# Kernel tuning notes

Hardware: AMD Instinct MI355X
Metric: run time of the kernel (lower is better)

## Reference

```python
import jax, jax.numpy as jnp
import numpy as np
from jax import lax

HID = 512
NEG = -1e30

def conv2d(x, w, pad):
    # x: [N,C,H,W], w: [O,I,kh,kw]
    return lax.conv_general_dilated(x, w, (1, 1), [(pad, pad), (pad, pad)],
                                    dimension_numbers=('NCHW', 'OIHW', 'NCHW'))

def maxpool3s2p1(x):
    return lax.reduce_window(x, -jnp.inf, lax.max, (1, 1, 3, 3), (1, 1, 2, 2),
                             [(0, 0), (0, 0), (1, 1), (1, 1)])

def setup_inputs() -> dict:
    key = jax.random.key(0)
    ks = jax.random.split(key, 12)
    N, B = 128, 16
    gid = jnp.repeat(jnp.arange(B), N // B).astype(jnp.float32)  # sorted group ids
    rois = jnp.concatenate([gid[:, None], jax.random.uniform(ks[0], (N, 4))], axis=1)
    interact_feat = jax.random.normal(ks[1], (N, 2304, 1, 16, 16), jnp.float32)
    bbox_feat = jax.random.normal(ks[2], (N, 1024, 4, 7, 7), jnp.float32)
    s = lambda k, sh: jax.random.normal(k, sh, jnp.float32) * 0.02
    return {
        'rois': rois,
        'interact_feat': interact_feat,
        'bbox_feat': bbox_feat,
        'w_reduce': s(ks[3], (HID, 2304, 1, 1)),
        'w_rsize': s(ks[4], (HID, HID, 3, 3)),
        'wq': s(ks[5], (HID, HID, 3, 3)),
        'wk': s(ks[6], (HID, HID, 3, 3)),
        'wv': s(ks[7], (HID, HID, 3, 3)),
        'w1': s(ks[8], (HID, HID, 3, 3)),
        'gamma': jnp.ones((HID,), jnp.float32),
        'beta': jnp.zeros((HID,), jnp.float32),
        'w_fc': s(ks[9], (HID, 2 * HID)),
    }

def reference(rois, interact_feat, bbox_feat, w_reduce, w_rsize, wq, wk, wv, w1, gamma, beta, w_fc):
    f = interact_feat[:, :, 0]                      # squeeze(2): [N,2304,16,16]
    f = jax.nn.relu(conv2d(f, w_reduce, 0))         # [N,512,16,16]
    f = conv2d(f, w_rsize, 0)                       # no padding -> [N,512,14,14]
    f = maxpool3s2p1(f)                             # [N,512,7,7]

    gid = rois[:, 0].astype(jnp.int32)
    mask = gid[:, None] == gid[None, :]             # [N,N] same-group mask (vectorizes ragged loop)

    q = conv2d(f, wq, 1)
    k = conv2d(f, wk, 1)
    v = conv2d(f, wv, 1)
    # per-pixel attention across rois within each group
    att = jnp.einsum('ichw,jchw->ijhw', q, k) / jnp.sqrt(jnp.asarray(HID, f.dtype))
    att = jnp.where(mask[:, :, None, None], att, NEG)
    att = jax.nn.softmax(att, axis=1)               # softmax over key rois (dim=1)
    virt = jnp.einsum('ijhw,jchw->ichw', att, v)    # [N,512,7,7]

    # GroupNorm(1, C): normalize over (C,H,W), per-channel affine
    mu = virt.mean(axis=(1, 2, 3), keepdims=True)
    var = virt.var(axis=(1, 2, 3), keepdims=True)
    virt = (virt - mu) / jnp.sqrt(var + 1e-5)
    virt = virt * gamma[None, :, None, None] + beta[None, :, None, None]
    virt = jax.nn.relu(virt)
    virt = conv2d(virt, w1, 1)                      # dropout = identity in eval

    ho = (f + virt).mean(axis=(2, 3))               # gap1 -> [N,512]
    ob = bbox_feat.mean(axis=(2, 3, 4))             # gap2 -> [N,1024]
    ob = jax.nn.relu(ob @ w_fc.T)                   # fc1 -> [N,512]
    return jnp.concatenate([ho, ob], axis=1)        # [N,1024]
```

## Files before the change

### kernel.cpp

```cpp
#include <hip/hip_runtime.h>
#include <hip/hip_bf16.h>
#include <math.h>

typedef __bf16 bf16;
typedef __bf16 v8bf __attribute__((ext_vector_type(8)));
typedef float f32x4 __attribute__((ext_vector_type(4)));

#define GLDS16(g, l) __builtin_amdgcn_global_load_lds( \
    (const __attribute__((address_space(1))) void*)(g), \
    (__attribute__((address_space(3))) void*)(l), 16, 0, 0)

__device__ __forceinline__ int xcd_swz(int bid, int nwg) {
  int xcd = bid & 7, off = bid >> 3;
  int q = nwg >> 3, r = nwg & 7;
  return (xcd < r ? xcd * (q + 1) : r * (q + 1) + (xcd - r) * q) + off;
}

#define RING_COMPUTE() do { \
  v8bf b_[4], a_[4]; \
  _Pragma("unroll") for (int _j = 0; _j < 4; ++_j) { \
    int _lr = _j * 16 + l15; \
    int _c = (wn * 64 + colb) ^ ((_lr & 7) << 4); \
    b_[_j] = *(const v8bf*)(s0 + 16384 + _lr * 128 + _c); } \
  _Pragma("unroll") for (int _i = 0; _i < 4; ++_i) { \
    int _lr = _i * 16 + l15; \
    int _c = (wm * 64 + colb) ^ ((_lr & 7) << 4); \
    a_[_i] = *(const v8bf*)(s0 + _lr * 128 + _c); } \
  __builtin_amdgcn_s_setprio(1); \
  _Pragma("unroll") for (int _i = 0; _i < 4; ++_i) \
  _Pragma("unroll") for (int _j = 0; _j < 4; ++_j) \
    acc[_i][_j] = __builtin_amdgcn_mfma_f32_16x16x32_bf16(a_[_i], b_[_j], acc[_i][_j], 0, 0, 0); \
  __builtin_amdgcn_s_setprio(0); \
  _Pragma("unroll") for (int _i = 0; _i < 4; ++_i) { \
    int _lr = (_i + 4) * 16 + l15; \
    int _c = (wm * 64 + colb) ^ ((_lr & 7) << 4); \
    a_[_i] = *(const v8bf*)(s0 + _lr * 128 + _c); } \
  __builtin_amdgcn_s_setprio(1); \
  _Pragma("unroll") for (int _i = 0; _i < 4; ++_i) \
  _Pragma("unroll") for (int _j = 0; _j < 4; ++_j) \
    acc[_i + 4][_j] = __builtin_amdgcn_mfma_f32_16x16x32_bf16(a_[_i], b_[_j], acc[_i + 4][_j], 0, 0, 0); \
  __builtin_amdgcn_s_setprio(0); \
} while (0)

#define RING_LOOP(NG, STAGE) do { \
  STAGE(0, s0); STAGE(1, s1); \
  for (int g = 0; g < (NG); ++g) { \
    if (g + 2 < (NG)) { STAGE(g + 2, s2); } \
    if (g + 2 < (NG))       asm volatile("s_waitcnt vmcnt(12)" ::: "memory"); \
    else if (g + 2 == (NG)) asm volatile("s_waitcnt vmcnt(6)" ::: "memory"); \
    else                    asm volatile("s_waitcnt vmcnt(0)" ::: "memory"); \
    __builtin_amdgcn_s_barrier(); \
    __builtin_amdgcn_sched_barrier(0); \
    RING_COMPUTE(); \
    __builtin_amdgcn_sched_barrier(0); \
    __builtin_amdgcn_s_barrier(); \
    char* _tmp = s0; s0 = s1; s1 = s2; s2 = _tmp; \
  } \
} while (0)

__global__ __launch_bounds__(256, 2)
void k_gemm_reduce(const bf16* __restrict__ A, const bf16* __restrict__ B,
                   bf16* __restrict__ f1, int mbase)
{
  __shared__ __attribute__((aligned(16))) char lds[73728];
  char *s0 = lds, *s1 = lds + 24576, *s2 = lds + 49152;
  const int s = xcd_swz(blockIdx.x, gridDim.x);
  const int by = s & 3, bx = s >> 2;
  const int t = threadIdx.x, lane = t & 63, w = t >> 6;
  const int wm = w >> 1, wn = w & 1;
  const int l15 = lane & 15, colb = (lane >> 4) << 4;
  const int tr = t >> 3;
  const int lb = ((t & 7) << 4) ^ ((tr & 7) << 4);
  const int hi = lb >> 6, kb = lb & 63;
  const int t16 = t * 16;
  const char* pa[4]; const char* pb[2];
  #pragma unroll
  for (int i = 0; i < 4; ++i)
    pa[i] = (const char*)A + (size_t)(bx * 256 + i * 32 + tr + hi * 128) * 4608 + kb;
  #pragma unroll
  for (int i = 0; i < 2; ++i)
    pb[i] = (const char*)B + (size_t)(by * 128 + i * 32 + tr + hi * 64) * 4608 + kb;
  #define SG(kt, ring) do { \
    _Pragma("unroll") for (int _i = 0; _i < 4; ++_i) \
      GLDS16(pa[_i] + (size_t)(kt) * 64, (ring) + _i * 4096 + t16); \
    _Pragma("unroll") for (int _i = 0; _i < 2; ++_i) \
      GLDS16(pb[_i] + (size_t)(kt) * 64, (ring) + 16384 + _i * 4096 + t16); } while (0)
  f32x4 acc[8][4] = {};
  RING_LOOP(72, SG);
  const int rbase = (lane >> 4) << 2, cl = lane & 15;
  #pragma unroll
  for (int i = 0; i < 8; ++i)
    #pragma unroll
    for (int j = 0; j < 4; ++j)
      #pragma unroll
      for (int r = 0; r < 4; ++r) {
        int row = mbase + bx * 256 + wm * 128 + i * 16 + rbase + r;
        int col = by * 128 + wn * 64 + j * 16 + cl;
        f1[(size_t)row * 512 + col] = (bf16)fmaxf(acc[i][j][r], 0.f);
      }
}

__global__ __launch_bounds__(256, 2)
void k_conv_rsize(const bf16* __restrict__ f1, const bf16* __restrict__ wt,
                  bf16* __restrict__ f14)
{
  __shared__ __attribute__((aligned(16))) char lds[73728];
  char *s0 = lds, *s1 = lds + 24576, *s2 = lds + 49152;
  const int s = xcd_swz(blockIdx.x, gridDim.x);
  const int by = s & 3, bx = s >> 2;
  const int t = threadIdx.x, lane = t & 63, w = t >> 6;
  const int wm = w >> 1, wn = w & 1;
  const int l15 = lane & 15, colb = (lane >> 4) << 4;
  const int tr = t >> 3;
  const int lb = ((t & 7) << 4) ^ ((tr & 7) << 4);
  const int hi = lb >> 6, kb = lb & 63;
  const int t16 = t * 16;
  int abase[4]; const char* pb[2];
  #pragma unroll
  for (int i = 0; i < 4; ++i) {
    int m = bx * 256 + i * 32 + tr + hi * 128;
    int n = m / 196, rem = m - n * 196;
    int y = rem / 14, x = rem - 14 * (rem / 14);
    abase[i] = n * 256 + y * 16 + x;
  }
  #pragma unroll
  for (int i = 0; i < 2; ++i)
    pb[i] = (const char*)wt + (size_t)(by * 128 + i * 32 + tr + hi * 64) * 1024 + kb;
  const char* f1c = (const char*)f1 + kb;
  #define SC(kt, ring) do { int _tap = (kt) >> 4, _ko = ((kt) & 15) << 6; \
    int _dy = (_tap * 11) >> 5, _dx = _tap - _dy * 3; \
    int _df = (_dy * 16 + _dx) << 10; \
    _Pragma("unroll") for (int _i = 0; _i < 4; ++_i) \
      GLDS16(f1c + ((size_t)abase[_i] << 10) + _df + _ko, (ring) + _i * 4096 + t16); \
    _Pragma("unroll") for (int _i = 0; _i < 2; ++_i) \
      GLDS16(pb[_i] + (size_t)_tap * 524288 + _ko, (ring) + 16384 + _i * 4096 + t16); } while (0)
  f32x4 acc[8][4] = {};
  RING_LOOP(144, SC);
  const int rbase = (lane >> 4) << 2, cl = lane & 15;
  #pragma unroll
  for (int i = 0; i < 8; ++i)
    #pragma unroll
    for (int j = 0; j < 4; ++j)
      #pragma unroll
      for (int r = 0; r < 4; ++r) {
        int row = bx * 256 + wm * 128 + i * 16 + rbase + r;
        int col = by * 128 + wn * 64 + j * 16 + cl;
        f14[(size_t)row * 512 + col] = (bf16)acc[i][j][r];
      }
}

__global__ __launch_bounds__(256, 2)
void k_conv_qkv(const bf16* __restrict__ fin, const bf16* __restrict__ wt,
                bf16* __restrict__ qkv, const bf16* __restrict__ zp,
                const float* __restrict__ bbox, float* __restrict__ obm)
{
  __shared__ __attribute__((aligned(16))) char lds[73728];
  char *s0 = lds, *s1 = lds + 24576, *s2 = lds + 49152;
  const int t = threadIdx.x;
  if (blockIdx.x >= 300) {
    int bid = blockIdx.x - 300;
    int n = bid >> 4;
    int c = (bid & 15) * 64 + (t >> 2);
    int seg = t & 3;
    const float4* p4 = (const float4*)(bbox + ((size_t)n * 1024 + c) * 196);
    float sum = 0.f;
    for (int k = seg; k < 49; k += 4) { float4 ww = p4[k]; sum += ww.x + ww.y + ww.z + ww.w; }
    sum += __shfl_xor(sum, 1);
    sum += __shfl_xor(sum, 2);
    if (seg == 0) obm[n * 1024 + c] = sum * (1.f / 196.f);
    return;
  }
  const int s = xcd_swz(blockIdx.x, 300);
  const int q12 = s % 12, bx = s / 12;
  const int tensor = q12 >> 2, byl = q12 & 3;
  const char* wtc = (const char*)wt + (size_t)tensor * 4718592;
  bf16* outp = qkv + (size_t)tensor * 3211264;
  const int lane = t & 63, w = t >> 6;
  const int wm = w >> 1, wn = w & 1;
  const int l15 = lane & 15, colb = (lane >> 4) << 4;
  const int tr = t >> 3;
  const int lb = ((t & 7) << 4) ^ ((tr & 7) << 4);
  const int hi = lb >> 6, kb = lb & 63;
  const int t16 = t * 16;
  int nb[4], py[4], px[4]; const char* pb[2];
  #pragma unroll
  for (int i = 0; i < 4; ++i) {
    int m = bx * 256 + i * 32 + tr + hi * 128;
    if (m > 6271) m = 6271;
    int n = m / 49, rem = m - n * 49;
    nb[i] = n * 49;
    py[i] = rem / 7 - 1;
    px[i] = rem - 7 * (rem / 7) - 1;
  }
  #pragma unroll
  for (int i = 0; i < 2; ++i)
    pb[i] = wtc + (size_t)(byl * 128 + i * 32 + tr + hi * 64) * 1024 + kb;
  const char* finc = (const char*)fin + kb;
  const char* zpc = (const char*)zp;
  #define SQ(kt, ring) do { int _tap = (kt) >> 4, _ko = ((kt) & 15) << 6; \
    int _dy = (_tap * 11) >> 5, _dx = _tap - _dy * 3; \
    _Pragma("unroll") for (int _i = 0; _i < 4; ++_i) { \
      int _iy = py[_i] + _dy, _ix = px[_i] + _dx; \
      const char* _sp = ((unsigned)_iy < 7u && (unsigned)_ix < 7u) \
          ? finc + (size_t)(nb[_i] + _iy * 7 + _ix) * 1024 + _ko : zpc; \
      GLDS16(_sp, (ring) + _i * 4096 + t16); } \
    _Pragma("unroll") for (int _i = 0; _i < 2; ++_i) \
      GLDS16(pb[_i] + (size_t)_tap * 524288 + _ko, (ring) + 16384 + _i * 4096 + t16); } while (0)
  f32x4 acc[8][4] = {};
  RING_LOOP(144, SQ);
  const int rbase = (lane >> 4) << 2, cl = lane & 15;
  #pragma unroll
  for (int i = 0; i < 8; ++i)
    #pragma unroll
    for (int j = 0; j < 4; ++j)
      #pragma unroll
      for (int r = 0; r < 4; ++r) {
        int row = bx * 256 + wm * 128 + i * 16 + rbase + r;
        if (row < 6272) {
          int col = byl * 128 + wn * 64 + j * 16 + cl;
          outp[(size_t)row * 512 + col] = (bf16)acc[i][j][r];
        }
      }
}

__device__ __forceinline__ void tile_compute(const char* ldsA, const char* ldsB,
                                             f32x4 (&acc)[4][4], int wr, int wc, int lane) {
  const int l15 = lane & 15;
  const int colb = (lane >> 4) << 4;
  #pragma unroll
  for (int kk = 0; kk < 2; ++kk) {
    v8bf a[4], b[4];
    #pragma unroll
    for (int i = 0; i < 4; ++i) {
      int ra = wr * 64 + i * 16 + l15;
      int ca = ((kk << 6) | colb) ^ ((ra & 7) << 4);
      a[i] = *(const v8bf*)(ldsA + ra * 128 + ca);
    }
    #pragma unroll
    for (int j = 0; j < 4; ++j) {
      int rb = wc * 64 + j * 16 + l15;
      int cb = ((kk << 6) | colb) ^ ((rb & 7) << 4);
      b[j] = *(const v8bf*)(ldsB + rb * 128 + cb);
    }
    __builtin_amdgcn_s_setprio(1);
    #pragma unroll
    for (int i = 0; i < 4; ++i)
      #pragma unroll
      for (int j = 0; j < 4; ++j)
        acc[i][j] = __builtin_amdgcn_mfma_f32_16x16x32_bf16(a[i], b[j], acc[i][j], 0, 0, 0);
    __builtin_amdgcn_s_setprio(0);
  }
}

#define PIPELINE_LOOP(NK)                                                   \
  stage(0, lds);                                                            \
  stage(1, lds + 32768);                                                    \
  int cur = 0;                                                              \
  for (int ks = 0; ks < (NK) - 1; ++ks) {                                   \
    asm volatile("s_waitcnt vmcnt(8)" ::: "memory");                        \
    __builtin_amdgcn_s_barrier();                                           \
    __builtin_amdgcn_sched_barrier(0);                                      \
    tile_compute(lds + cur * 32768, lds + cur * 32768 + 16384, acc, wr, wc, lane); \
    __builtin_amdgcn_sched_barrier(0);                                      \
    __builtin_amdgcn_s_barrier();                                           \
    __builtin_amdgcn_sched_barrier(0);                                      \
    if (ks + 2 < (NK)) stage(ks + 2, lds + cur * 32768);                    \
    cur ^= 1;                                                               \
  }                                                                         \
  asm volatile("s_waitcnt vmcnt(0)" ::: "memory");                          \
  __builtin_amdgcn_s_barrier();                                             \
  __builtin_amdgcn_sched_barrier(0);                                        \
  tile_compute(lds + cur * 32768, lds + cur * 32768 + 16384, acc, wr, wc, lane);

__global__ __launch_bounds__(256)
void k_gemm_s(const bf16* __restrict__ A_s, const bf16* __restrict__ w1r,
              float* __restrict__ part)
{
  __shared__ __attribute__((aligned(16))) char lds[65536];
  const int by = blockIdx.x, kspl = blockIdx.y;
  const int t = threadIdx.x, lane = t & 63, w = t >> 6, wr = w >> 1, wc = w & 1;
  const int tr = t >> 3;
  const int cphys = ((t & 7) << 4) ^ ((tr & 7) << 4);
  const char* pa[4]; const char* pb[4];
  #pragma unroll
  for (int i = 0; i < 4; ++i) {
    int r = i * 32 + tr;
    pa[i] = (const char*)A_s + (size_t)r * 9216 + kspl * 2304 + cphys;
    pb[i] = (const char*)w1r + (size_t)(by * 128 + r) * 9216 + kspl * 2304 + cphys;
  }
  const int lo = t * 16;
  auto stage = [&](int ks, char* base) {
    #pragma unroll
    for (int i = 0; i < 4; ++i) GLDS16(pa[i] + ks * 128, base + lo + i * 4096);
    #pragma unroll
    for (int i = 0; i < 4; ++i) GLDS16(pb[i] + ks * 128, base + 16384 + lo + i * 4096);
  };
  f32x4 acc[4][4] = {};
  PIPELINE_LOOP(18)
  const int rb = (lane >> 4) << 2, cl = lane & 15;
  #pragma unroll
  for (int i = 0; i < 4; ++i)
    #pragma unroll
    for (int j = 0; j < 4; ++j)
      #pragma unroll
      for (int r = 0; r < 4; ++r) {
        int row = wr * 64 + i * 16 + rb + r;
        int col = by * 128 + wc * 64 + j * 16 + cl;
        part[(size_t)kspl * 65536 + row * 512 + col] = acc[i][j][r];
      }
}

__global__ __launch_bounds__(512)
void k_red(const float* __restrict__ part, const float* __restrict__ f7m,
           float* __restrict__ out)
{
  int idx = blockIdx.x * 512 + threadIdx.x;
  float s = part[idx] + part[65536 + idx] + part[131072 + idx] + part[196608 + idx];
  int row = idx >> 9, col = idx & 511;
  out[row * 1024 + col] = s + f7m[idx];
}

__global__ void k_tin(const float* __restrict__ in, bf16* __restrict__ A1, int n0)
{
  __shared__ float tile[64][36];
  const int k0 = blockIdx.x * 64, p0 = blockIdx.y * 32, nl = blockIdx.z;
  const int n = n0 + nl;
  const int t = threadIdx.x;
  const float* src = in + (size_t)n * 2304 * 256;
  #pragma unroll
  for (int rep = 0; rep < 2; ++rep) {
    int idx = t + rep * 256;
    int row = idx >> 3, c4 = (idx & 7) * 4;
    float4 v = *(const float4*)(src + (size_t)(k0 + row) * 256 + p0 + c4);
    tile[row][c4] = v.x; tile[row][c4 + 1] = v.y;
    tile[row][c4 + 2] = v.z; tile[row][c4 + 3] = v.w;
  }
  __syncthreads();
  const int pl = t >> 3, ke = (t & 7) * 8;
  v8bf o;
  #pragma unroll
  for (int e = 0; e < 8; ++e) o[e] = (bf16)tile[ke + e][pl];
  bf16* dst = A1 + (size_t)nl * 256 * 2304;
  *(v8bf*)(dst + (size_t)(p0 + pl) * 2304 + k0 + ke) = o;
}

__global__ void k_castw(const float* __restrict__ wsrc, bf16* __restrict__ wb, int nelem)
{
  int idx = (blockIdx.x * 256 + threadIdx.x) * 4;
  if (idx >= nelem) return;
  float4 v = *(const float4*)(wsrc + idx);
  bf16 o0 = (bf16)v.x, o1 = (bf16)v.y, o2 = (bf16)v.z, o3 = (bf16)v.w;
  bf16* d = wb + idx;
  d[0] = o0; d[1] = o1; d[2] = o2; d[3] = o3;
}

__global__ void k_wtrans(const float* __restrict__ s0, const float* __restrict__ s1,
                         const float* __restrict__ s2, const float* __restrict__ s3,
                         const float* __restrict__ s4, bf16* __restrict__ wt,
                         bf16* __restrict__ w1r)
{
  const float* src;
  switch (blockIdx.y) {
    case 0: src = s0; break; case 1: src = s1; break; case 2: src = s2; break;
    case 3: src = s3; break; default: src = s4; break;
  }
  int q = blockIdx.x * 256 + threadIdx.x;
  const float* sp = src + (size_t)q * 9;
  float tmp[9];
  #pragma unroll
  for (int e = 0; e < 9; ++e) tmp[e] = sp[e];
  if (blockIdx.y < 4) {
    bf16* dst = wt + (size_t)blockIdx.y * 2359296;
    #pragma unroll
    for (int e = 0; e < 9; ++e) dst[(size_t)e * 262144 + q] = (bf16)tmp[e];
  } else {
    int co = q >> 9, ci = q & 511;
    #pragma unroll
    for (int e = 0; e < 9; ++e) w1r[(size_t)(co * 9 + e) * 512 + ci] = (bf16)tmp[e];
  }
}

__global__ void k_pool(const bf16* __restrict__ f14, bf16* __restrict__ f7b)
{
  int idx = blockIdx.x * 256 + threadIdx.x;
  int c2 = idx & 255;
  int pp = idx >> 8;
  int n = pp / 49, p7 = pp - n * 49;
  int y = p7 / 7, x = p7 - 7 * (p7 / 7);
  int y0 = 2 * y - 1, x0 = 2 * x - 1;
  const unsigned* f14u = (const unsigned*)f14;
  float m0 = -3.4e38f, m1 = -3.4e38f;
  #pragma unroll
  for (int dy = 0; dy < 3; ++dy) {
    int iy = y0 + dy; if ((unsigned)iy >= 14u) continue;
    #pragma unroll
    for (int dx = 0; dx < 3; ++dx) {
      int ix = x0 + dx; if ((unsigned)ix >= 14u) continue;
      unsigned vv = f14u[(size_t)(n * 196 + iy * 14 + ix) * 256 + c2];
      m0 = fmaxf(m0, __builtin_bit_cast(float, vv << 16));
      m1 = fmaxf(m1, __builtin_bit_cast(float, vv & 0xffff0000u));
    }
  }
  bf16 b0 = (bf16)m0, b1 = (bf16)m1;
  unsigned pk = (unsigned)__builtin_bit_cast(unsigned short, b0)
              | ((unsigned)__builtin_bit_cast(unsigned short, b1) << 16);
  ((unsigned*)f7b)[idx] = pk;
}

__global__ __launch_bounds__(256)
void k_attn(const bf16* __restrict__ q, const bf16* __restrict__ k,
            const bf16* __restrict__ v, const float* __restrict__ rois,
            float* __restrict__ virt)
{
  const int p = blockIdx.x, g = blockIdx.y, t = threadIdx.x;
  __shared__ float sS[8][9];
  __shared__ float sP[8][9];
  __shared__ __attribute__((aligned(16))) bf16 sV[8][512];
  {
    int u = t;
    #pragma unroll
    for (int rep = 0; rep < 2; ++rep, u += 256) {
      int j = u >> 6, ch = u & 63;
      *(v8bf*)&sV[j][ch * 8] = *(const v8bf*)(v + ((size_t)(g * 8 + j) * 49 + p) * 512 + ch * 8);
    }
  }
  int pi = t >> 2, ls = t & 3;
  int i = pi >> 3, j = pi & 7;
  const bf16* qi = q + ((size_t)(g * 8 + i) * 49 + p) * 512;
  const bf16* kj = k + ((size_t)(g * 8 + j) * 49 + p) * 512;
  float s = 0.f;
  for (int ch = ls * 16; ch < ls * 16 + 16; ++ch) {
    v8bf a = *(const v8bf*)(qi + ch * 8);
    v8bf b = *(const v8bf*)(kj + ch * 8);
    #pragma unroll
    for (int e = 0; e < 8; ++e) s += (float)a[e] * (float)b[e];
  }
  s += __shfl_xor(s, 1);
  s += __shfl_xor(s, 2);
  if (ls == 0) sS[i][j] = s * 0.04419417382415922f;
  __syncthreads();
  if (t < 8) {
    float gi = rois[(g * 8 + t) * 5];
    float pv[8]; float mx = -3.4e38f;
    #pragma unroll
    for (int jj = 0; jj < 8; ++jj) {
      float gj = rois[(g * 8 + jj) * 5];
      float sv = (gi == gj) ? sS[t][jj] : -1e30f;
      pv[jj] = sv; mx = fmaxf(mx, sv);
    }
    float sum = 0.f;
    #pragma unroll
    for (int jj = 0; jj < 8; ++jj) { float e = expf(pv[jj] - mx); pv[jj] = e; sum += e; }
    float inv = 1.f / sum;
    #pragma unroll
    for (int jj = 0; jj < 8; ++jj) sP[t][jj] = pv[jj] * inv;
  }
  __syncthreads();
  int i2 = t >> 5, c0 = (t & 31) * 16;
  float o[16];
  #pragma unroll
  for (int e = 0; e < 16; ++e) o[e] = 0.f;
  #pragma unroll
  for (int jj = 0; jj < 8; ++jj) {
    float ww = sP[i2][jj];
    v8bf v0 = *(const v8bf*)&sV[jj][c0];
    v8bf v1 = *(const v8bf*)&sV[jj][c0 + 8];
    #pragma unroll
    for (int e = 0; e < 8; ++e) { o[e] += ww * (float)v0[e]; o[8 + e] += ww * (float)v1[e]; }
  }
  float* dst = virt + ((size_t)(g * 8 + i2) * 49 + p) * 512 + c0;
  #pragma unroll
  for (int e = 0; e < 16; ++e) dst[e] = o[e];
}

__global__ __launch_bounds__(512)
void k_ln_fc(const float* __restrict__ virt, const float* __restrict__ gamma,
             const float* __restrict__ beta, const bf16* __restrict__ f7b,
             bf16* __restrict__ A_s, float* __restrict__ f7m,
             const float* __restrict__ obm, const float* __restrict__ wfc,
             float* __restrict__ out)
{
  const int t = threadIdx.x;
  if (blockIdx.x >= 128) {
    __shared__ float sO[1024];
    int n = blockIdx.x - 128;
    for (int u = t; u < 1024; u += 512) sO[u] = obm[n * 1024 + u];
    __syncthreads();
    const float4* wp = (const float4*)(wfc + (size_t)t * 1024);
    float s = 0.f;
    for (int c4 = 0; c4 < 256; ++c4) {
      float4 w = wp[c4];
      s += w.x * sO[c4 * 4] + w.y * sO[c4 * 4 + 1] + w.z * sO[c4 * 4 + 2] + w.w * sO[c4 * 4 + 3];
    }
    out[n * 1024 + 512 + t] = fmaxf(s, 0.f);
    return;
  }
  const int n = blockIdx.x;
  const float* p = virt + (size_t)n * 25088 + t;
  float xv[49];
  float s1 = 0.f, s2 = 0.f;
  #pragma unroll
  for (int pp = 0; pp < 49; ++pp) {
    float x = p[pp * 512];
    xv[pp] = x; s1 += x; s2 += x * x;
  }
  __shared__ float r1[512], r2[512];
  r1[t] = s1; r2[t] = s2; __syncthreads();
  for (int off = 256; off; off >>= 1) {
    if (t < off) { r1[t] += r1[t + off]; r2[t] += r2[t + off]; }
    __syncthreads();
  }
  float mu = r1[0] * (1.f / 25088.f);
  float var = r2[0] * (1.f / 25088.f) - mu * mu;
  float rstd = rsqrtf(var + 1e-5f);
  float g = gamma[t], be = beta[t];
  const bf16* fp = f7b + (size_t)n * 25088 + t;
  float T = 0, R0 = 0, R6 = 0, C0 = 0, C6 = 0;
  float X00 = 0, X06 = 0, X60 = 0, X66 = 0, F = 0;
  #pragma unroll
  for (int pp = 0; pp < 49; ++pp) {
    const int u = pp / 7, v = pp - 7 * (pp / 7);
    float y = fmaxf((xv[pp] - mu) * rstd * g + be, 0.f);
    T += y;
    if (u == 0) R0 += y;
    if (u == 6) R6 += y;
    if (v == 0) C0 += y;
    if (v == 6) C6 += y;
    if (pp == 0)  X00 = y;
    if (pp == 6)  X06 = y;
    if (pp == 42) X60 = y;
    if (pp == 48) X66 = y;
    F += (float)fp[pp * 512];
  }
  float sv[9] = { T-R6-C6+X66, T-R6, T-R6-C0+X60,
                  T-C6,        T,    T-C0,
                  T-R0-C6+X06, T-R0, T-R0-C0+X00 };
  bf16* Ap = A_s + (size_t)n * 4608 + t;
  #pragma unroll
  for (int tap = 0; tap < 9; ++tap)
    Ap[tap * 512] = (bf16)(sv[tap] * (1.f / 49.f));
  f7m[n * 512 + t] = F * (1.f / 49.f);
}

extern "C" void kernel_launch(void* const* d_in, const int* in_sizes, int n_in,
                              void* d_out, int out_size, void* d_ws, size_t ws_size,
                              hipStream_t stream) {
  const float* rois     = (const float*)d_in[0];
  const float* interact = (const float*)d_in[1];
  const float* bbox     = (const float*)d_in[2];
  const float* w_reduce = (const float*)d_in[3];
  const float* w_rsize  = (const float*)d_in[4];
  const float* wq       = (const float*)d_in[5];
  const float* wk       = (const float*)d_in[6];
  const float* wv       = (const float*)d_in[7];
  const float* w1       = (const float*)d_in[8];
  const float* gamma    = (const float*)d_in[9];
  const float* beta     = (const float*)d_in[10];
  const float* wfc      = (const float*)d_in[11];
  float* out = (float*)d_out;
  char* ws = (char*)d_ws;

  size_t o = 0;
  auto take = [&](size_t sz) { size_t r = o; o += (sz + 255) & ~(size_t)255; return r; };
  bf16*  wrb   = (bf16*)(ws + take(2359296));
  bf16*  wt    = (bf16*)(ws + take(18874368));
  bf16*  w1r   = (bf16*)(ws + take(4718592));
  char*  Rf1   = ws + take(33554432);
  bf16*  f7b   = (bf16*)(ws + take(6422528));
  float* virt  = (float*)(ws + take(12845056));
  bf16*  A_s   = (bf16*)(ws + take(1179648));
  float* f7m   = (float*)(ws + take(262144));
  float* part  = (float*)(ws + take(1048576));
  float* obm   = (float*)(ws + take(524288));
  bf16*  zp    = (bf16*)(ws + take(256));
  size_t fixedEnd = o;
  const size_t A1_FULL = 150994944;
  bool full = (ws_size >= fixedEnd + A1_FULL);
  bf16* A1  = (bf16*)(ws + fixedEnd);
  bf16* f14 = (bf16*)(ws + fixedEnd);

  bf16* f1 = (bf16*)Rf1;
  bf16* qb = (bf16*)Rf1;
  bf16* kb = qb + 3211264;
  bf16* vb = kb + 3211264;

  hipMemsetAsync(zp, 0, 256, stream);

  k_castw<<<1152, 256, 0, stream>>>(w_reduce, wrb, 1179648);
  k_wtrans<<<dim3(1024, 5), 256, 0, stream>>>(w_rsize, wq, wk, wv, w1, wt, w1r);

  if (full) {
    k_tin<<<dim3(36, 8, 128), 256, 0, stream>>>(interact, A1, 0);
    k_gemm_reduce<<<512, 256, 0, stream>>>(A1, wrb, f1, 0);
  } else {
    for (int ch = 0; ch < 4; ++ch) {
      k_tin<<<dim3(36, 8, 32), 256, 0, stream>>>(interact, A1, ch * 32);
      k_gemm_reduce<<<128, 256, 0, stream>>>(A1, wrb, f1, ch * 8192);
    }
  }

  k_conv_rsize<<<392, 256, 0, stream>>>(f1, wt, f14);
  k_pool<<<6272, 256, 0, stream>>>(f14, f7b);

  k_conv_qkv<<<2348, 256, 0, stream>>>(f7b, wt + (size_t)1 * 2359296, qb, zp, bbox, obm);

  k_attn<<<dim3(49, 16), 256, 0, stream>>>(qb, kb, vb, rois, virt);

  k_ln_fc<<<256, 512, 0, stream>>>(virt, gamma, beta, f7b, A_s, f7m, obm, wfc, out);

  k_gemm_s<<<dim3(4, 4), 256, 0, stream>>>(A_s, w1r, part);
  k_red<<<128, 512, 0, stream>>>(part, f7m, out);
}
```

Baseline: 543.0 us.

## Fuse input transpose-cast into reduce GEMM and merge weight prep kernels

The reduce GEMM now reads the fp32 NCHW interact features directly, converts them to bf16 in registers and writes them into swizzled LDS. This removes the separate transpose kernel and its large bf16 intermediate buffer round-trip. The pipeline drops from a 3-stage async ring to 2-stage double buffering with register staging for A, and the two weight-cast kernels are merged into one launch. In exchange, the A loads are strided scalar fp32 reads and there is less latency hiding, so the GEMM mainloop may slow down.

```diff
diff --git a/kernel.cpp b/kernel.cpp
--- a/kernel.cpp
+++ b/kernel.cpp
@@ -16,16 +16,16 @@
   return (xcd < r ? xcd * (q + 1) : r * (q + 1) + (xcd - r) * q) + off;
 }
 
-#define RING_COMPUTE() do { \
+#define RING_COMPUTE_P(SP) do { \
   v8bf b_[4], a_[4]; \
   _Pragma("unroll") for (int _j = 0; _j < 4; ++_j) { \
     int _lr = _j * 16 + l15; \
     int _c = (wn * 64 + colb) ^ ((_lr & 7) << 4); \
-    b_[_j] = *(const v8bf*)(s0 + 16384 + _lr * 128 + _c); } \
+    b_[_j] = *(const v8bf*)((SP) + 16384 + _lr * 128 + _c); } \
   _Pragma("unroll") for (int _i = 0; _i < 4; ++_i) { \
     int _lr = _i * 16 + l15; \
     int _c = (wm * 64 + colb) ^ ((_lr & 7) << 4); \
-    a_[_i] = *(const v8bf*)(s0 + _lr * 128 + _c); } \
+    a_[_i] = *(const v8bf*)((SP) + _lr * 128 + _c); } \
   __builtin_amdgcn_s_setprio(1); \
   _Pragma("unroll") for (int _i = 0; _i < 4; ++_i) \
   _Pragma("unroll") for (int _j = 0; _j < 4; ++_j) \
@@ -34,13 +34,15 @@
   _Pragma("unroll") for (int _i = 0; _i < 4; ++_i) { \
     int _lr = (_i + 4) * 16 + l15; \
     int _c = (wm * 64 + colb) ^ ((_lr & 7) << 4); \
-    a_[_i] = *(const v8bf*)(s0 + _lr * 128 + _c); } \
+    a_[_i] = *(const v8bf*)((SP) + _lr * 128 + _c); } \
   __builtin_amdgcn_s_setprio(1); \
   _Pragma("unroll") for (int _i = 0; _i < 4; ++_i) \
   _Pragma("unroll") for (int _j = 0; _j < 4; ++_j) \
     acc[_i + 4][_j] = __builtin_amdgcn_mfma_f32_16x16x32_bf16(a_[_i], b_[_j], acc[_i + 4][_j], 0, 0, 0); \
   __builtin_amdgcn_s_setprio(0); \
 } while (0)
+
+#define RING_COMPUTE() RING_COMPUTE_P(s0)
 
 #define RING_LOOP(NG, STAGE) do { \
   STAGE(0, s0); STAGE(1, s1); \
@@ -59,34 +61,58 @@
 } while (0)
 
 __global__ __launch_bounds__(256, 2)
-void k_gemm_reduce(const bf16* __restrict__ A, const bf16* __restrict__ B,
-                   bf16* __restrict__ f1, int mbase)
-{
-  __shared__ __attribute__((aligned(16))) char lds[73728];
-  char *s0 = lds, *s1 = lds + 24576, *s2 = lds + 49152;
+void k_gemm_reduce_f(const float* __restrict__ interact, const bf16* __restrict__ Bw,
+                     bf16* __restrict__ f1)
+{
+  __shared__ __attribute__((aligned(16))) char lds[49152];
   const int s = xcd_swz(blockIdx.x, gridDim.x);
-  const int by = s & 3, bx = s >> 2;
+  const int by = s & 3, n = s >> 2;
   const int t = threadIdx.x, lane = t & 63, w = t >> 6;
   const int wm = w >> 1, wn = w & 1;
   const int l15 = lane & 15, colb = (lane >> 4) << 4;
-  const int tr = t >> 3;
-  const int lb = ((t & 7) << 4) ^ ((tr & 7) << 4);
-  const int hi = lb >> 6, kb = lb & 63;
+  const int tr = t >> 3, s8 = t & 7;
+  const int lb = (s8 << 4) ^ ((tr & 7) << 4);
+  const int hi = lb >> 6, j8 = (lb >> 4) & 3;
   const int t16 = t * 16;
-  const char* pa[4]; const char* pb[2];
-  #pragma unroll
-  for (int i = 0; i < 4; ++i)
-    pa[i] = (const char*)A + (size_t)(bx * 256 + i * 32 + tr + hi * 128) * 4608 + kb;
+  const float* abase = interact + (size_t)n * 589824 + (size_t)(j8 * 8) * 256 + tr + hi * 128;
+  const char* pb[2];
   #pragma unroll
   for (int i = 0; i < 2; ++i)
-    pb[i] = (const char*)B + (size_t)(by * 128 + i * 32 + tr + hi * 64) * 4608 + kb;
-  #define SG(kt, ring) do { \
+    pb[i] = (const char*)Bw + (size_t)(by * 128 + i * 32 + tr + hi * 64) * 4608 + (lb & 63);
+
+  float ar[4][8];
+  #define ALOAD_R(kt) do { \
+    const float* _ab = abase + (size_t)(kt) * 8192; \
     _Pragma("unroll") for (int _i = 0; _i < 4; ++_i) \
-      GLDS16(pa[_i] + (size_t)(kt) * 64, (ring) + _i * 4096 + t16); \
-    _Pragma("unroll") for (int _i = 0; _i < 2; ++_i) \
-      GLDS16(pb[_i] + (size_t)(kt) * 64, (ring) + 16384 + _i * 4096 + t16); } while (0)
+    _Pragma("unroll") for (int _e = 0; _e < 8; ++_e) \
+      ar[_i][_e] = _ab[_e * 256 + _i * 32]; } while (0)
+  #define AWRITE_R(dst) do { \
+    _Pragma("unroll") for (int _i = 0; _i < 4; ++_i) { \
+      v8bf _o; \
+      _Pragma("unroll") for (int _e = 0; _e < 8; ++_e) _o[_e] = (bf16)ar[_i][_e]; \
+      *(v8bf*)((dst) + _i * 4096 + t16) = _o; } } while (0)
+  #define BGLDS_R(kt, dst) do { \
+    GLDS16(pb[0] + (size_t)(kt) * 64, (dst) + 16384 + t16); \
+    GLDS16(pb[1] + (size_t)(kt) * 64, (dst) + 16384 + 4096 + t16); } while (0)
+
   f32x4 acc[8][4] = {};
-  RING_LOOP(72, SG);
+  ALOAD_R(0);
+  BGLDS_R(0, lds);
+  int cur = 0;
+  for (int g = 0; g < 72; ++g) {
+    char* scur = lds + cur * 24576;
+    AWRITE_R(scur);
+    __builtin_amdgcn_sched_barrier(0);
+    if (g + 1 < 72) { ALOAD_R(g + 1); BGLDS_R(g + 1, lds + (cur ^ 1) * 24576); }
+    if (g + 1 < 72) asm volatile("s_waitcnt lgkmcnt(0) vmcnt(34)" ::: "memory");
+    else            asm volatile("s_waitcnt lgkmcnt(0) vmcnt(0)" ::: "memory");
+    __builtin_amdgcn_s_barrier();
+    __builtin_amdgcn_sched_barrier(0);
+    RING_COMPUTE_P(scur);
+    __builtin_amdgcn_sched_barrier(0);
+    __builtin_amdgcn_s_barrier();
+    cur ^= 1;
+  }
   const int rbase = (lane >> 4) << 2, cl = lane & 15;
   #pragma unroll
   for (int i = 0; i < 8; ++i)
@@ -94,7 +120,7 @@
     for (int j = 0; j < 4; ++j)
       #pragma unroll
       for (int r = 0; r < 4; ++r) {
-        int row = mbase + bx * 256 + wm * 128 + i * 16 + rbase + r;
+        int row = n * 256 + wm * 128 + i * 16 + rbase + r;
         int col = by * 128 + wn * 64 + j * 16 + cl;
         f1[(size_t)row * 512 + col] = (bf16)fmaxf(acc[i][j][r], 0.f);
       }
@@ -320,57 +346,33 @@
   out[row * 1024 + col] = s + f7m[idx];
 }
 
-__global__ void k_tin(const float* __restrict__ in, bf16* __restrict__ A1, int n0)
-{
-  __shared__ float tile[64][36];
-  const int k0 = blockIdx.x * 64, p0 = blockIdx.y * 32, nl = blockIdx.z;
-  const int n = n0 + nl;
-  const int t = threadIdx.x;
-  const float* src = in + (size_t)n * 2304 * 256;
-  #pragma unroll
-  for (int rep = 0; rep < 2; ++rep) {
-    int idx = t + rep * 256;
-    int row = idx >> 3, c4 = (idx & 7) * 4;
-    float4 v = *(const float4*)(src + (size_t)(k0 + row) * 256 + p0 + c4);
-    tile[row][c4] = v.x; tile[row][c4 + 1] = v.y;
-    tile[row][c4 + 2] = v.z; tile[row][c4 + 3] = v.w;
-  }
-  __syncthreads();
-  const int pl = t >> 3, ke = (t & 7) * 8;
-  v8bf o;
-  #pragma unroll
-  for (int e = 0; e < 8; ++e) o[e] = (bf16)tile[ke + e][pl];
-  bf16* dst = A1 + (size_t)nl * 256 * 2304;
-  *(v8bf*)(dst + (size_t)(p0 + pl) * 2304 + k0 + ke) = o;
-}
-
-__global__ void k_castw(const float* __restrict__ wsrc, bf16* __restrict__ wb, int nelem)
-{
-  int idx = (blockIdx.x * 256 + threadIdx.x) * 4;
-  if (idx >= nelem) return;
-  float4 v = *(const float4*)(wsrc + idx);
-  bf16 o0 = (bf16)v.x, o1 = (bf16)v.y, o2 = (bf16)v.z, o3 = (bf16)v.w;
-  bf16* d = wb + idx;
-  d[0] = o0; d[1] = o1; d[2] = o2; d[3] = o3;
-}
-
-__global__ void k_wtrans(const float* __restrict__ s0, const float* __restrict__ s1,
-                         const float* __restrict__ s2, const float* __restrict__ s3,
-                         const float* __restrict__ s4, bf16* __restrict__ wt,
-                         bf16* __restrict__ w1r)
-{
+__global__ void k_wprep(const float* __restrict__ wred, const float* __restrict__ s0,
+                        const float* __restrict__ s1, const float* __restrict__ s2,
+                        const float* __restrict__ s3, const float* __restrict__ s4,
+                        bf16* __restrict__ wrb, bf16* __restrict__ wt,
+                        bf16* __restrict__ w1r)
+{
+  if (blockIdx.x < 1152) {
+    int idx = (blockIdx.x * 256 + threadIdx.x) * 4;
+    float4 v = *(const float4*)(wred + idx);
+    bf16* d = wrb + idx;
+    d[0] = (bf16)v.x; d[1] = (bf16)v.y; d[2] = (bf16)v.z; d[3] = (bf16)v.w;
+    return;
+  }
+  int bid = blockIdx.x - 1152;
+  int by = bid >> 10, bx = bid & 1023;
   const float* src;
-  switch (blockIdx.y) {
+  switch (by) {
     case 0: src = s0; break; case 1: src = s1; break; case 2: src = s2; break;
     case 3: src = s3; break; default: src = s4; break;
   }
-  int q = blockIdx.x * 256 + threadIdx.x;
+  int q = bx * 256 + threadIdx.x;
   const float* sp = src + (size_t)q * 9;
   float tmp[9];
   #pragma unroll
   for (int e = 0; e < 9; ++e) tmp[e] = sp[e];
-  if (blockIdx.y < 4) {
-    bf16* dst = wt + (size_t)blockIdx.y * 2359296;
+  if (by < 4) {
+    bf16* dst = wt + (size_t)by * 2359296;
     #pragma unroll
     for (int e = 0; e < 9; ++e) dst[(size_t)e * 262144 + q] = (bf16)tmp[e];
   } else {
@@ -574,9 +576,6 @@
   float* obm   = (float*)(ws + take(524288));
   bf16*  zp    = (bf16*)(ws + take(256));
   size_t fixedEnd = o;
-  const size_t A1_FULL = 150994944;
-  bool full = (ws_size >= fixedEnd + A1_FULL);
-  bf16* A1  = (bf16*)(ws + fixedEnd);
   bf16* f14 = (bf16*)(ws + fixedEnd);
 
   bf16* f1 = (bf16*)Rf1;
@@ -586,18 +585,9 @@
 
   hipMemsetAsync(zp, 0, 256, stream);
 
-  k_castw<<<1152, 256, 0, stream>>>(w_reduce, wrb, 1179648);
-  k_wtrans<<<dim3(1024, 5), 256, 0, stream>>>(w_rsize, wq, wk, wv, w1, wt, w1r);
-
-  if (full) {
-    k_tin<<<dim3(36, 8, 128), 256, 0, stream>>>(interact, A1, 0);
-    k_gemm_reduce<<<512, 256, 0, stream>>>(A1, wrb, f1, 0);
-  } else {
-    for (int ch = 0; ch < 4; ++ch) {
-      k_tin<<<dim3(36, 8, 32), 256, 0, stream>>>(interact, A1, ch * 32);
-      k_gemm_reduce<<<128, 256, 0, stream>>>(A1, wrb, f1, ch * 8192);
-    }
-  }
+  k_wprep<<<6272, 256, 0, stream>>>(w_reduce, w_rsize, wq, wk, wv, w1, wrb, wt, w1r);
+
+  k_gemm_reduce_f<<<512, 256, 0, stream>>>(interact, wrb, f1);
 
   k_conv_rsize<<<392, 256, 0, stream>>>(f1, wt, f14);
   k_pool<<<6272, 256, 0, stream>>>(f14, f7b);
```

Measured after the change: 915.7 us. 68.6% more time.
